# Optimization experiments

Measured on AMD Instinct MI355X. Metric: run time of the kernel, lower is better.

Reference implementation:

```python
import jax, jax.numpy as jnp
import numpy as np

L, H, E, V = 8, 16, 1024, 32000   # n_layer, n_head, n_embd, vocab_size
B, T = 4, 1024                      # batch, block_size
HS = E // H                         # head_size = 64


def _ln(x, g, b, eps=1e-5):
    m = jnp.mean(x, axis=-1, keepdims=True)
    v = jnp.mean((x - m) ** 2, axis=-1, keepdims=True)
    return (x - m) / jnp.sqrt(v + eps) * g + b


def setup_inputs() -> dict:
    key = jax.random.key(0)
    ks = jax.random.split(key, 21)
    s = 0.02
    n = lambda k, shp: (jax.random.normal(k, shp, dtype=jnp.float32) * s)
    return {
        'idx': jax.random.randint(ks[0], (B, T), 0, V),
        'tok_emb': n(ks[1], (V, E)),
        'pos_emb': n(ks[2], (T, E)),
        'ln1_g': jnp.ones((L, E), jnp.float32),
        'ln1_b': jnp.zeros((L, E), jnp.float32),
        'Wq': n(ks[3], (L, E, E)),
        'Wk': n(ks[4], (L, E, E)),
        'Wv': n(ks[5], (L, E, E)),
        'Wo': n(ks[6], (L, E, E)),
        'bo': jnp.zeros((L, E), jnp.float32),
        'ln2_g': jnp.ones((L, E), jnp.float32),
        'ln2_b': jnp.zeros((L, E), jnp.float32),
        'W1': n(ks[7], (L, E, 4 * E)),
        'b1': jnp.zeros((L, 4 * E), jnp.float32),
        'W2': n(ks[8], (L, 4 * E, E)),
        'b2': jnp.zeros((L, E), jnp.float32),
        'lnf_g': jnp.ones((E,), jnp.float32),
        'lnf_b': jnp.zeros((E,), jnp.float32),
        'Wlm': n(ks[9], (E, V)),
        'blm': jnp.zeros((V,), jnp.float32),
    }


def reference(idx, tok_emb, pos_emb, ln1_g, ln1_b, Wq, Wk, Wv, Wo, bo,
              ln2_g, ln2_b, W1, b1, W2, b2, lnf_g, lnf_b, Wlm, blm):
    x = tok_emb[idx] + pos_emb[:T]               # [B, T, E]
    scale = E ** -0.5                            # NOTE: source scales by C=n_embd, not head_size
    mask = jnp.tril(jnp.ones((T, T), dtype=bool))
    for l in range(L):
        h = _ln(x, ln1_g[l], ln1_b[l])
        q = (h @ Wq[l]).reshape(B, T, H, HS).transpose(0, 2, 1, 3)   # [B,H,T,hs]
        k = (h @ Wk[l]).reshape(B, T, H, HS).transpose(0, 2, 1, 3)
        v = (h @ Wv[l]).reshape(B, T, H, HS).transpose(0, 2, 1, 3)
        att = jnp.einsum('bhqd,bhkd->bhqk', q, k) * scale
        att = jnp.where(mask, att, -jnp.inf)
        att = jax.nn.softmax(att, axis=-1)
        o = jnp.einsum('bhqk,bhkd->bhqd', att, v)
        o = o.transpose(0, 2, 1, 3).reshape(B, T, E)                 # concat heads
        x = x + o @ Wo[l] + bo[l]
        h2 = _ln(x, ln2_g[l], ln2_b[l])
        x = x + jax.nn.relu(h2 @ W1[l] + b1[l]) @ W2[l] + b2[l]
    x = _ln(x, lnf_g, lnf_b)
    return x @ Wlm + blm                          # logits [B, T, V]
```

## Files before the change

kernel.cpp:

```cpp
#include <hip/hip_runtime.h>
#include <math.h>

#define L_ 8
#define H_ 16
#define E_ 1024
#define V_ 32000
#define B_ 4
#define T_ 1024
#define HS_ 64
#define M_ 4096
#define QKVS_ 3072

typedef __attribute__((ext_vector_type(8))) short short8;
typedef __attribute__((ext_vector_type(4))) float f32x4;

__device__ __forceinline__ unsigned short f2bf(float f) {
  unsigned int u = __builtin_bit_cast(unsigned int, f);
  u += 0x7fffu + ((u >> 16) & 1u);
  return (unsigned short)(u >> 16);
}

__global__ __launch_bounds__(256) void k_embed(
    const int* __restrict__ idx, const float* __restrict__ tok,
    const float* __restrict__ pos, float* __restrict__ x) {
  int bt = blockIdx.x;
  int t  = bt & (T_ - 1);
  int token = idx[bt];
  const float4* te = (const float4*)(tok + (size_t)token * E_);
  const float4* pe = (const float4*)(pos + (size_t)t * E_);
  float4* xo = (float4*)(x + (size_t)bt * E_);
  int i = threadIdx.x;
  float4 a = te[i], b = pe[i];
  xo[i] = make_float4(a.x + b.x, a.y + b.y, a.z + b.z, a.w + b.w);
}

__global__ __launch_bounds__(256) void k_wt(
    const float* __restrict__ W, unsigned short* __restrict__ WT,
    int K, int N, size_t ss, size_t ds) {
  __shared__ unsigned short t[64][66];
  const float* Ws = W + (size_t)blockIdx.z * ss;
  unsigned short* Wd = WT + (size_t)blockIdx.z * ds;
  int n0 = blockIdx.x * 64, k0 = blockIdx.y * 64;
  int tid = threadIdx.x;
  int c = tid & 63, r4 = tid >> 6;
  #pragma unroll
  for (int i = 0; i < 16; ++i) {
    int kr = i * 4 + r4;
    t[kr][c] = f2bf(Ws[(size_t)(k0 + kr) * N + n0 + c]);
  }
  __syncthreads();
  #pragma unroll
  for (int i = 0; i < 16; ++i) {
    int nr = i * 4 + r4;
    Wd[(size_t)(n0 + nr) * K + k0 + c] = t[c][nr];
  }
}

__device__ __forceinline__ float blk_sum256(float v, float* red) {
  #pragma unroll
  for (int o = 1; o < 64; o <<= 1) v += __shfl_xor(v, o);
  int wid = threadIdx.x >> 6, lane = threadIdx.x & 63;
  if (lane == 0) red[wid] = v;
  __syncthreads();
  v = red[0] + red[1] + red[2] + red[3];
  __syncthreads();
  return v;
}

__global__ __launch_bounds__(256) void k_ln_bf(
    const float* __restrict__ X, const float* __restrict__ g,
    const float* __restrict__ b, unsigned short* __restrict__ Y) {
  __shared__ float red[4];
  int row = blockIdx.x;
  int i = threadIdx.x;
  float4 xv = ((const float4*)(X + (size_t)row * E_))[i];
  float s = xv.x + xv.y + xv.z + xv.w;
  s = blk_sum256(s, red);
  float mean = s * (1.0f / E_);
  float dx = xv.x - mean, dy = xv.y - mean, dz = xv.z - mean, dw = xv.w - mean;
  float vs = dx*dx + dy*dy + dz*dz + dw*dw;
  vs = blk_sum256(vs, red);
  float rstd = rsqrtf(vs * (1.0f / E_) + 1e-5f);
  float4 gv = ((const float4*)g)[i];
  float4 bv = ((const float4*)b)[i];
  ushort4 o;
  o.x = f2bf(dx * rstd * gv.x + bv.x);
  o.y = f2bf(dy * rstd * gv.y + bv.y);
  o.z = f2bf(dz * rstd * gv.z + bv.z);
  o.w = f2bf(dw * rstd * gv.w + bv.w);
  ((ushort4*)(Y + (size_t)row * E_))[i] = o;
}

#define BUFE 16384

#define GLDS(src, dst) __builtin_amdgcn_global_load_lds( \
    (const __attribute__((address_space(1))) void*)(src), \
    (__attribute__((address_space(3))) void*)(dst), 16, 0, 0)

#define BAR() do { asm volatile("" ::: "memory"); __builtin_amdgcn_s_barrier(); \
                   asm volatile("" ::: "memory"); } while (0)

template<int OT, bool RELU>
__global__ __launch_bounds__(512, 2) void k_gemm_256(
    const unsigned short* __restrict__ A, const unsigned short* __restrict__ BT,
    const float* __restrict__ bias, void* __restrict__ Cout, int N, int K) {
  __shared__ __attribute__((aligned(16))) unsigned short As[2 * BUFE];
  __shared__ __attribute__((aligned(16))) unsigned short Bs[2 * BUFE];
  int tid = threadIdx.x;
  int lane = tid & 63, w = tid >> 6;
  int lr = lane & 15, lq = (lane >> 4) & 3;
  int wm = w >> 2, wn = w & 3;

  int nwg = gridDim.x, orig = blockIdx.x;
  int qq = nwg >> 3, rr = nwg & 7;
  int xcd = orig & 7, lid = orig >> 3;
  int wg = (xcd < rr ? xcd * (qq + 1) : rr * (qq + 1) + (xcd - rr) * qq) + lid;
  int m0 = (wg & 15) * 256;
  int n0 = (wg >> 4) * 256;

  int srow = w * 8 + (lane >> 3);
  int skoff = ((lane & 7) ^ (lane >> 3)) * 8;
  const unsigned short* aS = A + (size_t)(m0 + srow) * K + skoff;
  const unsigned short* bS = BT + (size_t)(n0 + srow) * K + skoff;

#define STG_A(boff, half, tt) { \
  GLDS(aS + (size_t)((half) * 128) * K + (tt) * 64,        &As[(boff) + (((half) * 128) << 6) + (w << 9)]); \
  GLDS(aS + (size_t)((half) * 128 + 64) * K + (tt) * 64,   &As[(boff) + (((half) * 128 + 64) << 6) + (w << 9)]); }
#define STG_B(boff, half, tt) { \
  GLDS(bS + (size_t)((half) * 128) * K + (tt) * 64,        &Bs[(boff) + (((half) * 128) << 6) + (w << 9)]); \
  GLDS(bS + (size_t)((half) * 128 + 64) * K + (tt) * 64,   &Bs[(boff) + (((half) * 128 + 64) << 6) + (w << 9)]); }
#define LDA_(dst, mh, ks) { _Pragma("unroll") for (int m_ = 0; m_ < 4; ++m_) \
  dst[m_] = *(const short8*)&As[so + ((wm * 128 + (mh) * 64 + m_ * 16 + lr) << 6) + ((((ks) * 4 + lq) ^ (lr & 7)) << 3)]; }
#define LDB_(dst, ks) { _Pragma("unroll") for (int n_ = 0; n_ < 4; ++n_) \
  dst[n_] = *(const short8*)&Bs[so + ((wn * 64 + n_ * 16 + lr) << 6) + ((((ks) * 4 + lq) ^ (lr & 7)) << 3)]; }
#define MMA(afr, mofs) do { __builtin_amdgcn_s_setprio(1); \
  _Pragma("unroll") for (int m_ = 0; m_ < 4; ++m_) { \
    _Pragma("unroll") for (int n_ = 0; n_ < 4; ++n_) \
      acc[(mofs) + m_][n_] = __builtin_amdgcn_mfma_f32_16x16x32_bf16(afr[m_], bfr[n_], acc[(mofs) + m_][n_], 0, 0, 0); } \
  __builtin_amdgcn_s_setprio(0); } while (0)

  f32x4 acc[8][4] = {};
  const int NT = K >> 6;

  STG_A(0, 0, 0); STG_A(0, 1, 0); STG_B(0, 0, 0); STG_B(0, 1, 0);
  if (NT > 1) {
    STG_B(BUFE, 0, 1);
    asm volatile("s_waitcnt vmcnt(2)" ::: "memory");
  } else {
    asm volatile("s_waitcnt vmcnt(0)" ::: "memory");
  }
  BAR();

  for (int t = 0; t < NT; ++t) {
    const int so = (t & 1) * BUFE;
    const int nbuf = ((t + 1) & 1) * BUFE;
    short8 af0[4], af1[4], bfr[4];
    LDA_(af0, 0, 0);
    LDB_(bfr, 0);
    if (t + 1 < NT) { STG_B(nbuf, 1, t + 1); }
    BAR();
    MMA(af0, 0);
    BAR();
    LDA_(af1, 1, 0);
    if (t + 1 < NT) { STG_A(nbuf, 0, t + 1); }
    BAR();
    MMA(af1, 4);
    BAR();
    LDA_(af0, 0, 1);
    LDB_(bfr, 1);
    if (t + 1 < NT) { STG_A(nbuf, 1, t + 1); }
    BAR();
    MMA(af0, 0);
    BAR();
    LDA_(af1, 1, 1);
    if (t + 2 < NT) { STG_B(so, 0, t + 2); }
    BAR();
    MMA(af1, 4);
    if (t + 2 < NT) { asm volatile("s_waitcnt vmcnt(2)" ::: "memory"); }
    else            { asm volatile("s_waitcnt vmcnt(0)" ::: "memory"); }
    BAR();
  }

  #pragma unroll
  for (int m = 0; m < 8; ++m) {
    #pragma unroll
    for (int n = 0; n < 4; ++n) {
      int col = n0 + wn * 64 + n * 16 + lr;
      float bv = bias ? bias[col] : 0.0f;
      #pragma unroll
      for (int i = 0; i < 4; ++i) {
        size_t row = (size_t)(m0 + wm * 128 + m * 16 + lq * 4 + i);
        float v = acc[m][n][i] + bv;
        if (RELU) v = fmaxf(v, 0.0f);
        if (OT == 0) ((float*)Cout)[row * N + col] = v;
        else ((unsigned short*)Cout)[row * N + col] = f2bf(v);
      }
    }
  }
#undef STG_A
#undef STG_B
#undef LDA_
#undef LDB_
#undef MMA
}

template<int BN, int OT, bool RELU, bool RES>
__global__ __launch_bounds__(256) void k_gemm_tn(
    const unsigned short* __restrict__ A, const unsigned short* __restrict__ BT,
    const float* __restrict__ bias, const float* __restrict__ R,
    void* __restrict__ Cout, int M, int N, int K) {
  constexpr int NF = BN / 32;
  __shared__ __attribute__((aligned(16))) unsigned short As[128 * 64];
  __shared__ __attribute__((aligned(16))) unsigned short Bs[BN * 64];
  int tid = threadIdx.x;
  int lane = tid & 63, w = tid >> 6;
  int lr = lane & 15, lq = lane >> 4;
  int m0 = blockIdx.x * 128, n0 = blockIdx.y * BN;
  int wr = (w >> 1) * 64, wc = (w & 1) * (BN / 2);

  int srow = w * 8 + (lane >> 3);
  int skoff = ((lane & 7) ^ (lane >> 3)) * 8;
  const unsigned short* a0 = A + (size_t)(m0 + srow) * K + skoff;
  const unsigned short* b0 = BT + (size_t)(n0 + srow) * K + skoff;

  f32x4 acc[4][NF] = {};

  for (int k0 = 0; k0 < K; k0 += 64) {
    __syncthreads();
    #pragma unroll
    for (int j = 0; j < 4; ++j)
      __builtin_amdgcn_global_load_lds(
          (const __attribute__((address_space(1))) void*)(a0 + (size_t)(j * 32) * K + k0),
          (__attribute__((address_space(3))) void*)(As + j * 2048 + w * 512), 16, 0, 0);
    #pragma unroll
    for (int j = 0; j < NF; ++j)
      __builtin_amdgcn_global_load_lds(
          (const __attribute__((address_space(1))) void*)(b0 + (size_t)(j * 32) * K + k0),
          (__attribute__((address_space(3))) void*)(Bs + j * 2048 + w * 512), 16, 0, 0);
    __syncthreads();
    short8 af[4][2], bf[NF][2];
    #pragma unroll
    for (int m = 0; m < 4; ++m)
      #pragma unroll
      for (int ks = 0; ks < 2; ++ks)
        af[m][ks] = *(const short8*)&As[(wr + m * 16 + lr) * 64 + (((ks * 4 + lq) ^ (lr & 7)) << 3)];
    #pragma unroll
    for (int n = 0; n < NF; ++n)
      #pragma unroll
      for (int ks = 0; ks < 2; ++ks)
        bf[n][ks] = *(const short8*)&Bs[(wc + n * 16 + lr) * 64 + (((ks * 4 + lq) ^ (lr & 7)) << 3)];
    #pragma unroll
    for (int ks = 0; ks < 2; ++ks)
      #pragma unroll
      for (int m = 0; m < 4; ++m)
        #pragma unroll
        for (int n = 0; n < NF; ++n)
          acc[m][n] = __builtin_amdgcn_mfma_f32_16x16x32_bf16(af[m][ks], bf[n][ks], acc[m][n], 0, 0, 0);
  }

  #pragma unroll
  for (int m = 0; m < 4; ++m) {
    #pragma unroll
    for (int n = 0; n < NF; ++n) {
      int col = n0 + wc + n * 16 + lr;
      float bv = bias ? bias[col] : 0.0f;
      #pragma unroll
      for (int i = 0; i < 4; ++i) {
        size_t row = (size_t)(m0 + wr + m * 16 + lq * 4 + i);
        float v = acc[m][n][i] + bv;
        if (RELU) v = fmaxf(v, 0.0f);
        if (RES)  v += R[row * N + col];
        if (OT == 0) ((float*)Cout)[row * N + col] = v;
        else ((unsigned short*)Cout)[row * N + col] = f2bf(v);
      }
    }
  }
}

template<int OT, bool RELU, bool RES>
__global__ __launch_bounds__(256) void k_gemm_bf(
    const unsigned short* __restrict__ A, const float* __restrict__ W,
    const float* __restrict__ bias, const float* __restrict__ R,
    void* __restrict__ Cout, int M, int N, int K) {
  __shared__ unsigned short As[128][40];
  __shared__ unsigned short Bs[128][40];
  int tid = threadIdx.x;
  int lane = tid & 63, wid = tid >> 6;
  int m0 = blockIdx.x * 128, n0 = blockIdx.y * 128;
  int wr = (wid >> 1) * 64, wc = (wid & 1) * 64;
  f32x4 acc[4][4] = {};
  int a_row = tid >> 1, a_koff = (tid & 1) * 16;
  int b_nb = tid & 31, b_kb = (tid >> 5) * 4;
  int lr = lane & 15, lq = lane >> 4;
  for (int k0 = 0; k0 < K; k0 += 32) {
    const unsigned short* ap = A + (size_t)(m0 + a_row) * K + k0 + a_koff;
    uint4 av0 = *(const uint4*)ap;
    uint4 av1 = *(const uint4*)(ap + 8);
    float wv[4][4];
    #pragma unroll
    for (int dk = 0; dk < 4; ++dk) {
      const float* wrow = W + (size_t)(k0 + b_kb + dk) * N + n0 + b_nb;
      #pragma unroll
      for (int j = 0; j < 4; ++j) wv[j][dk] = wrow[32 * j];
    }
    __syncthreads();
    *(uint4*)&As[a_row][a_koff]     = av0;
    *(uint4*)&As[a_row][a_koff + 8] = av1;
    #pragma unroll
    for (int j = 0; j < 4; ++j) {
      ushort4 pk;
      pk.x = f2bf(wv[j][0]); pk.y = f2bf(wv[j][1]);
      pk.z = f2bf(wv[j][2]); pk.w = f2bf(wv[j][3]);
      *(ushort4*)&Bs[b_nb + 32 * j][b_kb] = pk;
    }
    __syncthreads();
    short8 af[4], bf[4];
    #pragma unroll
    for (int m = 0; m < 4; ++m) af[m] = *(const short8*)&As[wr + m * 16 + lr][lq * 8];
    #pragma unroll
    for (int n = 0; n < 4; ++n) bf[n] = *(const short8*)&Bs[wc + n * 16 + lr][lq * 8];
    #pragma unroll
    for (int m = 0; m < 4; ++m)
      #pragma unroll
      for (int n = 0; n < 4; ++n)
        acc[m][n] = __builtin_amdgcn_mfma_f32_16x16x32_bf16(af[m], bf[n], acc[m][n], 0, 0, 0);
  }
  #pragma unroll
  for (int m = 0; m < 4; ++m) {
    #pragma unroll
    for (int n = 0; n < 4; ++n) {
      int col = n0 + wc + n * 16 + lr;
      float bv = bias ? bias[col] : 0.0f;
      #pragma unroll
      for (int i = 0; i < 4; ++i) {
        size_t row = (size_t)(m0 + wr + m * 16 + lq * 4 + i);
        float v = acc[m][n][i] + bv;
        if (RELU) v = fmaxf(v, 0.0f);
        if (RES)  v += R[row * N + col];
        if (OT == 0) ((float*)Cout)[row * N + col] = v;
        else ((unsigned short*)Cout)[row * N + col] = f2bf(v);
      }
    }
  }
}

__global__ __launch_bounds__(256) void k_fattn(
    const unsigned short* __restrict__ QKV, unsigned short* __restrict__ O) {
  __shared__ unsigned short Ks[64][72];
  __shared__ unsigned short Vs[64][74];
  __shared__ unsigned short Pl[4][32][72];
  int tid = threadIdx.x;
  int lane = tid & 63, wid = tid >> 6;
  int lr = lane & 15, lq = lane >> 4;
  int qt = blockIdx.x, bh = blockIdx.y;
  int b = bh >> 4, h = bh & 15;
  size_t base = ((size_t)b * T_) * QKVS_ + h * HS_;
  int q0w = qt * 128 + wid * 32;

  short8 qf[2][2];
  #pragma unroll
  for (int g = 0; g < 2; ++g)
    #pragma unroll
    for (int s = 0; s < 2; ++s)
      qf[g][s] = *(const short8*)(QKV + base + (size_t)(q0w + g * 16 + lr) * QKVS_ + s * 32 + lq * 8);

  f32x4 o_acc[2][4] = {};
  float mrun[2][4], lrun[2][4];
  #pragma unroll
  for (int g = 0; g < 2; ++g)
    #pragma unroll
    for (int i = 0; i < 4; ++i) { mrun[g][i] = -1e30f; lrun[g][i] = 0.0f; }
  const float sc = 0.03125f * 1.44269504f;
  int r = tid >> 2, cc = (tid & 3) * 16;
  int ntiles = 2 * qt + 2;

  for (int t = 0; t < ntiles; ++t) {
    __syncthreads();
    const unsigned short* kp = QKV + base + 1024 + (size_t)(t * 64 + r) * QKVS_ + cc;
    const unsigned short* vp = kp + 1024;
    uint4 k0v = *(const uint4*)kp, k1v = *(const uint4*)(kp + 8);
    uint4 v0v = *(const uint4*)vp, v1v = *(const uint4*)(vp + 8);
    *(uint4*)&Ks[r][cc] = k0v;
    *(uint4*)&Ks[r][cc + 8] = k1v;
    unsigned short vt[16];
    *(uint4*)&vt[0] = v0v; *(uint4*)&vt[8] = v1v;
    #pragma unroll
    for (int j = 0; j < 16; ++j) Vs[cc + j][r] = vt[j];
    __syncthreads();

    f32x4 sa[2][4] = {};
    #pragma unroll
    for (int nt = 0; nt < 4; ++nt)
      #pragma unroll
      for (int s = 0; s < 2; ++s) {
        short8 kf = *(const short8*)&Ks[nt * 16 + lr][s * 32 + lq * 8];
        sa[0][nt] = __builtin_amdgcn_mfma_f32_16x16x32_bf16(qf[0][s], kf, sa[0][nt], 0, 0, 0);
        sa[1][nt] = __builtin_amdgcn_mfma_f32_16x16x32_bf16(qf[1][s], kf, sa[1][nt], 0, 0, 0);
      }

    bool diag = (t >= 2 * qt);
    float p[2][4][4];
    #pragma unroll
    for (int g = 0; g < 2; ++g)
      #pragma unroll
      for (int nt = 0; nt < 4; ++nt)
        #pragma unroll
        for (int i = 0; i < 4; ++i) {
          float v = sa[g][nt][i] * sc;
          if (diag && (t * 64 + nt * 16 + lr > q0w + g * 16 + lq * 4 + i)) v = -1e30f;
          p[g][nt][i] = v;
        }
    #pragma unroll
    for (int g = 0; g < 2; ++g)
      #pragma unroll
      for (int i = 0; i < 4; ++i) {
        float v = fmaxf(fmaxf(p[g][0][i], p[g][1][i]), fmaxf(p[g][2][i], p[g][3][i]));
        #pragma unroll
        for (int o = 1; o < 16; o <<= 1) v = fmaxf(v, __shfl_xor(v, o));
        float mn = fmaxf(mrun[g][i], v);
        float corr = __builtin_amdgcn_exp2f(mrun[g][i] - mn);
        mrun[g][i] = mn;
        float ps = 0.0f;
        #pragma unroll
        for (int nt = 0; nt < 4; ++nt) {
          float pe = __builtin_amdgcn_exp2f(p[g][nt][i] - mn);
          p[g][nt][i] = pe;
          ps += pe;
        }
        lrun[g][i] = lrun[g][i] * corr + ps;
        #pragma unroll
        for (int dn = 0; dn < 4; ++dn) o_acc[g][dn][i] *= corr;
      }
    #pragma unroll
    for (int g = 0; g < 2; ++g)
      #pragma unroll
      for (int nt = 0; nt < 4; ++nt)
        #pragma unroll
        for (int i = 0; i < 4; ++i)
          Pl[wid][g * 16 + lq * 4 + i][nt * 16 + lr] = f2bf(p[g][nt][i]);
    __syncthreads();

    #pragma unroll
    for (int s = 0; s < 2; ++s) {
      short8 pa0 = *(const short8*)&Pl[wid][lr][s * 32 + lq * 8];
      short8 pa1 = *(const short8*)&Pl[wid][16 + lr][s * 32 + lq * 8];
      #pragma unroll
      for (int dn = 0; dn < 4; ++dn) {
        short8 vf = *(const short8*)&Vs[dn * 16 + lr][s * 32 + lq * 8];
        o_acc[0][dn] = __builtin_amdgcn_mfma_f32_16x16x32_bf16(pa0, vf, o_acc[0][dn], 0, 0, 0);
        o_acc[1][dn] = __builtin_amdgcn_mfma_f32_16x16x32_bf16(pa1, vf, o_acc[1][dn], 0, 0, 0);
      }
    }
  }

  #pragma unroll
  for (int g = 0; g < 2; ++g)
    #pragma unroll
    for (int i = 0; i < 4; ++i) {
      float v = lrun[g][i];
      #pragma unroll
      for (int o = 1; o < 16; o <<= 1) v += __shfl_xor(v, o);
      lrun[g][i] = 1.0f / v;
    }
  #pragma unroll
  for (int g = 0; g < 2; ++g)
    #pragma unroll
    for (int dn = 0; dn < 4; ++dn)
      #pragma unroll
      for (int i = 0; i < 4; ++i) {
        size_t row = (size_t)(b * T_) + q0w + g * 16 + lq * 4 + i;
        O[row * E_ + h * HS_ + dn * 16 + lr] = f2bf(o_acc[g][dn][i] * lrun[g][i]);
      }
}

extern "C" void kernel_launch(void* const* d_in, const int* in_sizes, int n_in,
                              void* d_out, int out_size, void* d_ws, size_t ws_size,
                              hipStream_t stream) {
  const int*   idx  = (const int*)d_in[0];
  const float* tok  = (const float*)d_in[1];
  const float* pos  = (const float*)d_in[2];
  const float* ln1g = (const float*)d_in[3];
  const float* ln1b = (const float*)d_in[4];
  const float* Wq   = (const float*)d_in[5];
  const float* Wk   = (const float*)d_in[6];
  const float* Wv   = (const float*)d_in[7];
  const float* Wo   = (const float*)d_in[8];
  const float* bo   = (const float*)d_in[9];
  const float* ln2g = (const float*)d_in[10];
  const float* ln2b = (const float*)d_in[11];
  const float* W1   = (const float*)d_in[12];
  const float* b1   = (const float*)d_in[13];
  const float* W2   = (const float*)d_in[14];
  const float* b2   = (const float*)d_in[15];
  const float* lnfg = (const float*)d_in[16];
  const float* lnfb = (const float*)d_in[17];
  const float* Wlm  = (const float*)d_in[18];
  const float* blm  = (const float*)d_in[19];

  char* scr = (char*)d_out;
  const size_t MB = 1024 * 1024;
  float*          xf    = (float*)(scr);
  unsigned short* qkvb  = (unsigned short*)(scr + 16 * MB);
  unsigned short* ob    = (unsigned short*)(scr + 40 * MB);
  unsigned short* mh    = (unsigned short*)(scr + 48 * MB);
  unsigned short* wqkvT = (unsigned short*)(scr + 80 * MB);
  unsigned short* woT   = (unsigned short*)(scr + 128 * MB);
  unsigned short* w1T   = (unsigned short*)(scr + 144 * MB);
  unsigned short* w2T   = (unsigned short*)(scr + 208 * MB);
  unsigned short* hb    = (unsigned short*)d_ws;
  unsigned short* wlmT  = (unsigned short*)((char*)d_ws + 8 * MB);
  const size_t EE = (size_t)E_ * E_;
  bool lm_fast = ws_size >= 8 * MB + (size_t)V_ * E_ * 2 + 1024;

  k_embed<<<M_, 256, 0, stream>>>(idx, tok, pos, xf);

  k_wt<<<dim3(16, 16, L_), 256, 0, stream>>>(Wq, wqkvT,          E_, E_, EE, 3 * EE);
  k_wt<<<dim3(16, 16, L_), 256, 0, stream>>>(Wk, wqkvT + EE,     E_, E_, EE, 3 * EE);
  k_wt<<<dim3(16, 16, L_), 256, 0, stream>>>(Wv, wqkvT + 2 * EE, E_, E_, EE, 3 * EE);
  k_wt<<<dim3(16, 16, L_), 256, 0, stream>>>(Wo, woT,            E_, E_, EE, EE);
  k_wt<<<dim3(64, 16, L_), 256, 0, stream>>>(W1, w1T, E_, 4 * E_, 4 * EE, 4 * EE);
  k_wt<<<dim3(16, 64, L_), 256, 0, stream>>>(W2, w2T, 4 * E_, E_, 4 * EE, 4 * EE);
  if (lm_fast)
    k_wt<<<dim3(V_ / 64, 16, 1), 256, 0, stream>>>(Wlm, wlmT, E_, V_, 0, 0);

  for (int l = 0; l < L_; ++l) {
    k_ln_bf<<<M_, 256, 0, stream>>>(xf, ln1g + l * E_, ln1b + l * E_, hb);
    k_gemm_256<1, false><<<16 * (QKVS_ / 256), 512, 0, stream>>>(
        hb, wqkvT + (size_t)l * 3 * EE, nullptr, qkvb, QKVS_, E_);
    k_fattn<<<dim3(T_ / 128, B_ * H_), 256, 0, stream>>>(qkvb, ob);
    k_gemm_tn<64, 0, false, true><<<dim3(32, 16), 256, 0, stream>>>(
        ob, woT + (size_t)l * EE, bo + l * E_, xf, xf, M_, E_, E_);
    k_ln_bf<<<M_, 256, 0, stream>>>(xf, ln2g + l * E_, ln2b + l * E_, hb);
    k_gemm_256<1, true><<<16 * (4 * E_ / 256), 512, 0, stream>>>(
        hb, w1T + (size_t)l * 4 * EE, b1 + (size_t)l * 4 * E_, mh, 4 * E_, E_);
    k_gemm_tn<64, 0, false, true><<<dim3(32, 16), 256, 0, stream>>>(
        mh, w2T + (size_t)l * 4 * EE, b2 + l * E_, xf, xf, M_, E_, 4 * E_);
  }
  k_ln_bf<<<M_, 256, 0, stream>>>(xf, lnfg, lnfb, hb);
  if (lm_fast)
    k_gemm_256<0, false><<<16 * (V_ / 256), 512, 0, stream>>>(
        hb, wlmT, blm, (float*)d_out, V_, E_);
  else
    k_gemm_bf<0, false, false><<<dim3(32, V_ / 128), 256, 0, stream>>>(
        hb, Wlm, blm, nullptr, (float*)d_out, M_, V_, E_);
}
```

Before: 2.644 ms.

## Split-K the FFN down-projection on 256-tile GEMM, prefetch attention K/V, reorder LM-head tiles

Moves the W2 GEMM (K=4096, N=1024) from the 128-row tn kernel to the 256x256 GEMM with a 4-way split-K, so 256 workgroups run instead of 64. Each split writes fp32 partials, and a new reduction kernel sums them with the bias and the residual. It also register-prefetches the next K/V tile in flash attention so global loads overlap the MFMA work. It switches the LM-head tile mapping to row-major over N. The cost is extra fp32 partial-sum traffic (64MB written and read) and one more launch per layer.

```diff
diff --git a/kernel.cpp b/kernel.cpp
--- a/kernel.cpp
+++ b/kernel.cpp
@@ -91,6 +91,24 @@
   ((ushort4*)(Y + (size_t)row * E_))[i] = o;
 }
 
+__global__ __launch_bounds__(256) void k_red4(
+    const float* __restrict__ p, const float* __restrict__ bias,
+    float* __restrict__ xf) {
+  const int ME = M_ * E_;
+  int i = blockIdx.x * 1024 + threadIdx.x * 4;
+  float4 a = *(const float4*)(p + i);
+  float4 b = *(const float4*)(p + ME + i);
+  float4 c = *(const float4*)(p + 2 * ME + i);
+  float4 d = *(const float4*)(p + 3 * ME + i);
+  float4 bv = *(const float4*)(bias + (i & (E_ - 1)));
+  float4 x = *(float4*)(xf + i);
+  x.x += a.x + b.x + c.x + d.x + bv.x;
+  x.y += a.y + b.y + c.y + d.y + bv.y;
+  x.z += a.z + b.z + c.z + d.z + bv.z;
+  x.w += a.w + b.w + c.w + d.w + bv.w;
+  *(float4*)(xf + i) = x;
+}
+
 #define BUFE 16384
 
 #define GLDS(src, dst) __builtin_amdgcn_global_load_lds( \
@@ -100,10 +118,10 @@
 #define BAR() do { asm volatile("" ::: "memory"); __builtin_amdgcn_s_barrier(); \
                    asm volatile("" ::: "memory"); } while (0)
 
-template<int OT, bool RELU>
+template<int OT, bool RELU, int DEC>
 __global__ __launch_bounds__(512, 2) void k_gemm_256(
     const unsigned short* __restrict__ A, const unsigned short* __restrict__ BT,
-    const float* __restrict__ bias, void* __restrict__ Cout, int N, int K) {
+    const float* __restrict__ bias, void* __restrict__ Cout, int N, int K, int Kstr) {
   __shared__ __attribute__((aligned(16))) unsigned short As[2 * BUFE];
   __shared__ __attribute__((aligned(16))) unsigned short Bs[2 * BUFE];
   int tid = threadIdx.x;
@@ -115,20 +133,29 @@
   int qq = nwg >> 3, rr = nwg & 7;
   int xcd = orig & 7, lid = orig >> 3;
   int wg = (xcd < rr ? xcd * (qq + 1) : rr * (qq + 1) + (xcd - rr) * qq) + lid;
-  int m0 = (wg & 15) * 256;
-  int n0 = (wg >> 4) * 256;
+  int m0, n0, kofs = 0;
+  size_t cofs = 0;
+  if constexpr (DEC == 0) { m0 = (wg & 15) * 256; n0 = (wg >> 4) * 256; }
+  else if constexpr (DEC == 1) { int nbn = N >> 8; m0 = (wg / nbn) * 256; n0 = (wg % nbn) * 256; }
+  else {
+    int inner = wg & 63;
+    m0 = (inner & 15) * 256; n0 = (inner >> 4) * 256;
+    int ks = wg >> 6;
+    kofs = ks * K;
+    cofs = (size_t)ks * M_ * (size_t)N;
+  }
 
   int srow = w * 8 + (lane >> 3);
   int skoff = ((lane & 7) ^ (lane >> 3)) * 8;
-  const unsigned short* aS = A + (size_t)(m0 + srow) * K + skoff;
-  const unsigned short* bS = BT + (size_t)(n0 + srow) * K + skoff;
+  const unsigned short* aS = A + (size_t)(m0 + srow) * Kstr + kofs + skoff;
+  const unsigned short* bS = BT + (size_t)(n0 + srow) * Kstr + kofs + skoff;
 
 #define STG_A(boff, half, tt) { \
-  GLDS(aS + (size_t)((half) * 128) * K + (tt) * 64,        &As[(boff) + (((half) * 128) << 6) + (w << 9)]); \
-  GLDS(aS + (size_t)((half) * 128 + 64) * K + (tt) * 64,   &As[(boff) + (((half) * 128 + 64) << 6) + (w << 9)]); }
+  GLDS(aS + (size_t)((half) * 128) * Kstr + (tt) * 64,        &As[(boff) + (((half) * 128) << 6) + (w << 9)]); \
+  GLDS(aS + (size_t)((half) * 128 + 64) * Kstr + (tt) * 64,   &As[(boff) + (((half) * 128 + 64) << 6) + (w << 9)]); }
 #define STG_B(boff, half, tt) { \
-  GLDS(bS + (size_t)((half) * 128) * K + (tt) * 64,        &Bs[(boff) + (((half) * 128) << 6) + (w << 9)]); \
-  GLDS(bS + (size_t)((half) * 128 + 64) * K + (tt) * 64,   &Bs[(boff) + (((half) * 128 + 64) << 6) + (w << 9)]); }
+  GLDS(bS + (size_t)((half) * 128) * Kstr + (tt) * 64,        &Bs[(boff) + (((half) * 128) << 6) + (w << 9)]); \
+  GLDS(bS + (size_t)((half) * 128 + 64) * Kstr + (tt) * 64,   &Bs[(boff) + (((half) * 128 + 64) << 6) + (w << 9)]); }
 #define LDA_(dst, mh, ks) { _Pragma("unroll") for (int m_ = 0; m_ < 4; ++m_) \
   dst[m_] = *(const short8*)&As[so + ((wm * 128 + (mh) * 64 + m_ * 16 + lr) << 6) + ((((ks) * 4 + lq) ^ (lr & 7)) << 3)]; }
 #define LDB_(dst, ks) { _Pragma("unroll") for (int n_ = 0; n_ < 4; ++n_) \
@@ -192,8 +219,8 @@
         size_t row = (size_t)(m0 + wm * 128 + m * 16 + lq * 4 + i);
         float v = acc[m][n][i] + bv;
         if (RELU) v = fmaxf(v, 0.0f);
-        if (OT == 0) ((float*)Cout)[row * N + col] = v;
-        else ((unsigned short*)Cout)[row * N + col] = f2bf(v);
+        if (OT == 0) ((float*)Cout)[cofs + row * N + col] = v;
+        else ((unsigned short*)Cout)[cofs + row * N + col] = f2bf(v);
       }
     }
   }
@@ -374,19 +401,27 @@
   int r = tid >> 2, cc = (tid & 3) * 16;
   int ntiles = 2 * qt + 2;
 
+  uint4 kA0, kA1, vA0, vA1;
+  {
+    const unsigned short* kp = QKV + base + 1024 + (size_t)r * QKVS_ + cc;
+    kA0 = *(const uint4*)kp; kA1 = *(const uint4*)(kp + 8);
+    vA0 = *(const uint4*)(kp + 1024); vA1 = *(const uint4*)(kp + 1032);
+  }
+
   for (int t = 0; t < ntiles; ++t) {
     __syncthreads();
-    const unsigned short* kp = QKV + base + 1024 + (size_t)(t * 64 + r) * QKVS_ + cc;
-    const unsigned short* vp = kp + 1024;
-    uint4 k0v = *(const uint4*)kp, k1v = *(const uint4*)(kp + 8);
-    uint4 v0v = *(const uint4*)vp, v1v = *(const uint4*)(vp + 8);
-    *(uint4*)&Ks[r][cc] = k0v;
-    *(uint4*)&Ks[r][cc + 8] = k1v;
+    *(uint4*)&Ks[r][cc] = kA0;
+    *(uint4*)&Ks[r][cc + 8] = kA1;
     unsigned short vt[16];
-    *(uint4*)&vt[0] = v0v; *(uint4*)&vt[8] = v1v;
+    *(uint4*)&vt[0] = vA0; *(uint4*)&vt[8] = vA1;
     #pragma unroll
     for (int j = 0; j < 16; ++j) Vs[cc + j][r] = vt[j];
     __syncthreads();
+    if (t + 1 < ntiles) {
+      const unsigned short* kp = QKV + base + 1024 + (size_t)((t + 1) * 64 + r) * QKVS_ + cc;
+      kA0 = *(const uint4*)kp; kA1 = *(const uint4*)(kp + 8);
+      vA0 = *(const uint4*)(kp + 1024); vA1 = *(const uint4*)(kp + 1032);
+    }
 
     f32x4 sa[2][4] = {};
     #pragma unroll
@@ -507,6 +542,7 @@
   unsigned short* woT   = (unsigned short*)(scr + 128 * MB);
   unsigned short* w1T   = (unsigned short*)(scr + 144 * MB);
   unsigned short* w2T   = (unsigned short*)(scr + 208 * MB);
+  float*          p2    = (float*)(scr + 280 * MB);
   unsigned short* hb    = (unsigned short*)d_ws;
   unsigned short* wlmT  = (unsigned short*)((char*)d_ws + 8 * MB);
   const size_t EE = (size_t)E_ * E_;
@@ -525,21 +561,22 @@
 
   for (int l = 0; l < L_; ++l) {
     k_ln_bf<<<M_, 256, 0, stream>>>(xf, ln1g + l * E_, ln1b + l * E_, hb);
-    k_gemm_256<1, false><<<16 * (QKVS_ / 256), 512, 0, stream>>>(
-        hb, wqkvT + (size_t)l * 3 * EE, nullptr, qkvb, QKVS_, E_);
+    k_gemm_256<1, false, 0><<<16 * (QKVS_ / 256), 512, 0, stream>>>(
+        hb, wqkvT + (size_t)l * 3 * EE, nullptr, qkvb, QKVS_, E_, E_);
     k_fattn<<<dim3(T_ / 128, B_ * H_), 256, 0, stream>>>(qkvb, ob);
     k_gemm_tn<64, 0, false, true><<<dim3(32, 16), 256, 0, stream>>>(
         ob, woT + (size_t)l * EE, bo + l * E_, xf, xf, M_, E_, E_);
     k_ln_bf<<<M_, 256, 0, stream>>>(xf, ln2g + l * E_, ln2b + l * E_, hb);
-    k_gemm_256<1, true><<<16 * (4 * E_ / 256), 512, 0, stream>>>(
-        hb, w1T + (size_t)l * 4 * EE, b1 + (size_t)l * 4 * E_, mh, 4 * E_, E_);
-    k_gemm_tn<64, 0, false, true><<<dim3(32, 16), 256, 0, stream>>>(
-        mh, w2T + (size_t)l * 4 * EE, b2 + l * E_, xf, xf, M_, E_, 4 * E_);
+    k_gemm_256<1, true, 0><<<16 * (4 * E_ / 256), 512, 0, stream>>>(
+        hb, w1T + (size_t)l * 4 * EE, b1 + (size_t)l * 4 * E_, mh, 4 * E_, E_, E_);
+    k_gemm_256<0, false, 2><<<256, 512, 0, stream>>>(
+        mh, w2T + (size_t)l * 4 * EE, nullptr, p2, E_, E_, 4 * E_);
+    k_red4<<<M_ * E_ / 1024, 256, 0, stream>>>(p2, b2 + l * E_, xf);
   }
   k_ln_bf<<<M_, 256, 0, stream>>>(xf, lnfg, lnfb, hb);
   if (lm_fast)
-    k_gemm_256<0, false><<<16 * (V_ / 256), 512, 0, stream>>>(
-        hb, wlmT, blm, (float*)d_out, V_, E_);
+    k_gemm_256<0, false, 1><<<16 * (V_ / 256), 512, 0, stream>>>(
+        hb, wlmT, blm, (float*)d_out, V_, E_, E_);
   else
     k_gemm_bf<0, false, false><<<dim3(32, V_ / 128), 256, 0, stream>>>(
         hb, Wlm, blm, nullptr, (float*)d_out, M_, V_, E_);
```

New measurement: 2.546 ms. -3.7%, faster.
